# Performance work log

Measured on AMD Instinct MI355X. Metric: run time of the kernel, lower is better.

Reference implementation:

```python
import jax, jax.numpy as jnp
import numpy as np

N = 100000
E = 1600000
NFEAT, NHID, NCLASS = 128, 128, 64


def setup_inputs() -> dict:
    key = jax.random.key(0)
    ks = jax.random.split(key, 8)
    x = jax.random.normal(ks[0], (N, NFEAT), dtype=jnp.float32)
    edge_index = jax.random.randint(ks[1], (2, E), 0, N, dtype=jnp.int32)
    def glorot(k, fan_in, fan_out):
        s = (6.0 / (fan_in + fan_out)) ** 0.5
        return jax.random.uniform(k, (fan_in, fan_out), jnp.float32, -s, s)
    W0 = glorot(ks[2], NFEAT, NHID)
    b0 = jnp.zeros((NHID,), jnp.float32)
    W1 = glorot(ks[3], NHID, NHID)
    b1 = jnp.zeros((NHID,), jnp.float32)
    W2 = glorot(ks[4], NHID, NCLASS)
    b2 = jnp.zeros((NCLASS,), jnp.float32)
    return {"x": x, "edge_index": edge_index, "W0": W0, "b0": b0,
            "W1": W1, "b1": b1, "W2": W2, "b2": b2}


def _normalized_adj(edge_index):
    # add self-loops (SparseTensor.set_diag)
    loops = jnp.arange(N, dtype=edge_index.dtype)
    row = jnp.concatenate([edge_index[0], loops])
    col = jnp.concatenate([edge_index[1], loops])
    ones = jnp.ones(row.shape[0], jnp.float32)
    deg = jax.ops.segment_sum(ones, row, num_segments=N)  # row sums incl. self-loop
    dis = jnp.where(deg > 0, deg ** -0.5, 0.0)
    w = dis[row] * dis[col]  # DAD: D^-1/2 A D^-1/2
    return row, col, w


def _spmm(row, col, w, h):
    # A @ h via gather + segment-sum: [E+N, d] intermediate
    return jax.ops.segment_sum(w[:, None] * h[col], row, num_segments=N)


def reference(x, edge_index, W0, b0, W1, b1, W2, b2):
    row, col, w = _normalized_adj(edge_index)
    h = x
    for Wl, bl, last in ((W0, b0, False), (W1, b1, False), (W2, b2, True)):
        h = _spmm(row, col, w, h @ Wl) + bl  # GCNConv(normalize=False)
        if not last:
            h = jax.nn.relu(h)  # dropout p=0.0 -> identity
    return h
```

## Files before the change

kernel.cpp:

```cpp
#include <hip/hip_runtime.h>


typedef __attribute__((ext_vector_type(8))) short bf16x8;
typedef __attribute__((ext_vector_type(4))) float floatx4;


__device__ inline unsigned short f2bf(float f) {
    union { float f; unsigned u; } v; v.f = f;
    unsigned r = v.u + 0x7fffu + ((v.u >> 16) & 1u);
    return (unsigned short)(r >> 16);
}

__device__ inline float bf2f(unsigned short h) {
    union { unsigned u; float f; } v; v.u = (unsigned)h << 16;
    return v.f;
}

__device__ inline void split_bf(float v, unsigned short& h, unsigned short& l) {
    h = f2bf(v);
    l = f2bf(v - bf2f(h));
}

__device__ inline void bf2x_to_f(unsigned u, float& a, float& b) {
    union { unsigned x; float f; } lo, hi;
    lo.x = u << 16; hi.x = u & 0xffff0000u;
    a = lo.f; b = hi.f;
}

__device__ inline void add8(float* acc, uint4 u) {
    float a, b;
    bf2x_to_f(u.x, a, b); acc[0] += a; acc[1] += b;
    bf2x_to_f(u.y, a, b); acc[2] += a; acc[3] += b;
    bf2x_to_f(u.z, a, b); acc[4] += a; acc[5] += b;
    bf2x_to_f(u.w, a, b); acc[6] += a; acc[7] += b;
}


__global__ void k_count(const int* __restrict__ row, int* __restrict__ deg,
                        int* __restrict__ pos, int e) {
    int i = blockIdx.x * blockDim.x + threadIdx.x;
    if (i < e) pos[i] = atomicAdd(&deg[row[i]], 1);
}

__global__ void k_dis(const int* __restrict__ deg, float* __restrict__ dis, int n) {
    int i = blockIdx.x * blockDim.x + threadIdx.x;
    if (i < n) dis[i] = rsqrtf((float)(deg[i] + 1));
}

__global__ void k_scan1(const int* __restrict__ deg, int* __restrict__ rp,
                        int* __restrict__ bsum, int n) {
    __shared__ int s[256];
    int tid = threadIdx.x;
    int i = blockIdx.x * 256 + tid;
    int v = (i < n) ? deg[i] : 0;
    s[tid] = v;
    __syncthreads();
    for (int off = 1; off < 256; off <<= 1) {
        int t = (tid >= off) ? s[tid - off] : 0;
        __syncthreads();
        s[tid] += t;
        __syncthreads();
    }
    if (i < n) rp[i] = s[tid] - v;
    if (tid == 255) bsum[blockIdx.x] = s[255];
}

__global__ void k_scan2(const int* __restrict__ bsum, int* __restrict__ boffs,
                        int nb, int* __restrict__ rp, int n, int total) {
    __shared__ int s[512];
    int tid = threadIdx.x;
    int v = (tid < nb) ? bsum[tid] : 0;
    s[tid] = v;
    __syncthreads();
    for (int off = 1; off < 512; off <<= 1) {
        int t = (tid >= off) ? s[tid - off] : 0;
        __syncthreads();
        s[tid] += t;
        __syncthreads();
    }
    if (tid < nb) boffs[tid] = s[tid] - v;
    if (tid == 0) rp[n] = total;
}

__global__ void k_scan3(int* __restrict__ rp, const int* __restrict__ boffs, int n) {
    int i = blockIdx.x * blockDim.x + threadIdx.x;
    if (i < n) rp[i] += boffs[i >> 8];
}

__global__ void k_scatter(const int* __restrict__ row, const int* __restrict__ col,
                          const int* __restrict__ rp, const int* __restrict__ pos,
                          int* __restrict__ csr, int e) {
    int i = blockIdx.x * blockDim.x + threadIdx.x;
    if (i < e) {
        int r = row[i];
        csr[rp[r] + pos[i]] = col[i];
    }
}


__global__ void k_prepX(const float* __restrict__ X, unsigned short* __restrict__ Xhi,
                        unsigned short* __restrict__ Xlo, int total4) {
    int id = blockIdx.x * blockDim.x + threadIdx.x;
    if (id < total4) {
        float4 v = ((const float4*)X)[id];
        ushort4 h, l;
        split_bf(v.x, h.x, l.x);
        split_bf(v.y, h.y, l.y);
        split_bf(v.z, h.z, l.z);
        split_bf(v.w, h.w, l.w);
        ((ushort4*)Xhi)[id] = h;
        ((ushort4*)Xlo)[id] = l;
    }
}

__global__ void k_prepW(const float* __restrict__ W, unsigned short* __restrict__ Wthi,
                        unsigned short* __restrict__ Wtlo, int ldw) {
    int id = blockIdx.x * blockDim.x + threadIdx.x;
    if (id < 128 * ldw) {
        int k = id / ldw, nn = id - k * ldw;
        unsigned short h, l;
        split_bf(W[id], h, l);
        Wthi[nn * 128 + k] = h;
        Wtlo[nn * 128 + k] = l;
    }
}


template <int NB>
__global__ __launch_bounds__(256) void k_gemm_mfma(
    const unsigned short* __restrict__ Ahi, const unsigned short* __restrict__ Alo,
    const unsigned short* __restrict__ Wthi, const unsigned short* __restrict__ Wtlo,
    const float* __restrict__ dis, unsigned short* __restrict__ T, int n) {
    const int LDW = NB * 64;
    __shared__ unsigned short Ah_s[64 * 128];
    __shared__ unsigned short Al_s[64 * 128];
    const int tid = threadIdx.x;
    const int bid = blockIdx.x;
    const int bx = (NB == 2) ? (bid >> 1) : bid;
    const int by = (NB == 2) ? (bid & 1) : 0;
    const int row0 = bx * 64;
    const int col0 = by * 64;

    const int wave = tid >> 6, lane = tid & 63;
    const int ln = lane & 15, quad = lane >> 4;
    const int m0 = (wave >> 1) * 32;
    const int nq0 = (wave & 1) * 32;

    bf16x8 Bh[4][2], Bl[4][2];
#pragma unroll
    for (int s = 0; s < 4; s++)
#pragma unroll
        for (int j = 0; j < 2; j++) {
            int ncol = col0 + nq0 + 16 * j + ln;
            int koff = 32 * s + quad * 8;
            Bh[s][j] = *(const bf16x8*)&Wthi[ncol * 128 + koff];
            Bl[s][j] = *(const bf16x8*)&Wtlo[ncol * 128 + koff];
        }

#pragma unroll
    for (int k = 0; k < 4; k++) {
        int id = k * 256 + tid;
        int r = id >> 4, c = id & 15;
        int gr = row0 + r;
        uint4 vh = make_uint4(0, 0, 0, 0), vl = make_uint4(0, 0, 0, 0);
        if (gr < n) {
            vh = *(const uint4*)&Ahi[(size_t)gr * 128 + c * 8];
            vl = *(const uint4*)&Alo[(size_t)gr * 128 + c * 8];
        }
        int pc = c ^ (r & 15);
        *(uint4*)&Ah_s[r * 128 + pc * 8] = vh;
        *(uint4*)&Al_s[r * 128 + pc * 8] = vl;
    }
    __syncthreads();

    floatx4 acc[2][2];
#pragma unroll
    for (int i = 0; i < 2; i++)
#pragma unroll
        for (int j = 0; j < 2; j++) acc[i][j] = (floatx4){0.f, 0.f, 0.f, 0.f};

#pragma unroll
    for (int s = 0; s < 4; s++) {
        bf16x8 ah[2], al[2];
#pragma unroll
        for (int i = 0; i < 2; i++) {
            int off = (m0 + 16 * i + ln) * 128 + ((4 * s + quad) ^ ln) * 8;
            ah[i] = *(const bf16x8*)&Ah_s[off];
            al[i] = *(const bf16x8*)&Al_s[off];
        }
#pragma unroll
        for (int i = 0; i < 2; i++)
#pragma unroll
            for (int j = 0; j < 2; j++) {
                acc[i][j] = __builtin_amdgcn_mfma_f32_16x16x32_bf16(
                    ah[i], Bh[s][j], acc[i][j], 0, 0, 0);
                acc[i][j] = __builtin_amdgcn_mfma_f32_16x16x32_bf16(
                    ah[i], Bl[s][j], acc[i][j], 0, 0, 0);
                acc[i][j] = __builtin_amdgcn_mfma_f32_16x16x32_bf16(
                    al[i], Bh[s][j], acc[i][j], 0, 0, 0);
            }
    }

#pragma unroll
    for (int i = 0; i < 2; i++)
#pragma unroll
        for (int reg = 0; reg < 4; reg++) {
            int gr = row0 + m0 + 16 * i + quad * 4 + reg;
            if (gr < n) {
                float ds = dis[gr];
#pragma unroll
                for (int j = 0; j < 2; j++) {
                    int gc = col0 + nq0 + 16 * j + ln;
                    T[(size_t)gr * LDW + gc] = f2bf(ds * acc[i][j][reg]);
                }
            }
        }
}


__global__ void k_agg128(const unsigned short* __restrict__ T,
                         unsigned short* __restrict__ Ohi,
                         unsigned short* __restrict__ Olo,
                         const int* __restrict__ rp, const int* __restrict__ cols,
                         const float* __restrict__ dis, const float* __restrict__ bias,
                         int n) {
    int wid = (blockIdx.x * blockDim.x + threadIdx.x) >> 6;
    int lane = threadIdx.x & 63;
    if (wid >= n) return;
    const int quad = lane >> 4;
    const int fl = (lane & 15) * 8;
    int beg = rp[wid], end = rp[wid + 1];

    float acc[8] = {0.f, 0.f, 0.f, 0.f, 0.f, 0.f, 0.f, 0.f};
    int e = beg + quad;
    for (; e + 12 < end; e += 16) {
        int c0 = cols[e];
        int c1 = cols[e + 4];
        int c2 = cols[e + 8];
        int c3 = cols[e + 12];
        uint4 u0 = *(const uint4*)&T[(size_t)c0 * 128 + fl];
        uint4 u1 = *(const uint4*)&T[(size_t)c1 * 128 + fl];
        uint4 u2 = *(const uint4*)&T[(size_t)c2 * 128 + fl];
        uint4 u3 = *(const uint4*)&T[(size_t)c3 * 128 + fl];
        add8(acc, u0);
        add8(acc, u1);
        add8(acc, u2);
        add8(acc, u3);
    }
    for (; e < end; e += 4) {
        int c = cols[e];
        uint4 u = *(const uint4*)&T[(size_t)c * 128 + fl];
        add8(acc, u);
    }
#pragma unroll
    for (int k = 0; k < 8; k++) {
        acc[k] += __shfl_xor(acc[k], 16);
        acc[k] += __shfl_xor(acc[k], 32);
    }
    if (quad == 0) {
        uint4 us = *(const uint4*)&T[(size_t)wid * 128 + fl];
        add8(acc, us);
        float di = dis[wid];
        float4 bA = *(const float4*)&bias[fl];
        float4 bB = *(const float4*)&bias[fl + 4];
        float bb[8] = {bA.x, bA.y, bA.z, bA.w, bB.x, bB.y, bB.z, bB.w};
        unsigned short h[8], l[8];
#pragma unroll
        for (int k = 0; k < 8; k++) {
            float o = fmaf(di, acc[k], bb[k]);
            o = fmaxf(o, 0.f);
            split_bf(o, h[k], l[k]);
        }
        ushort4 h0 = {h[0], h[1], h[2], h[3]}, h1 = {h[4], h[5], h[6], h[7]};
        ushort4 l0 = {l[0], l[1], l[2], l[3]}, l1 = {l[4], l[5], l[6], l[7]};
        *(ushort4*)&Ohi[(size_t)wid * 128 + fl] = h0;
        *(ushort4*)&Ohi[(size_t)wid * 128 + fl + 4] = h1;
        *(ushort4*)&Olo[(size_t)wid * 128 + fl] = l0;
        *(ushort4*)&Olo[(size_t)wid * 128 + fl + 4] = l1;
    }
}

__global__ void k_agg64(const unsigned short* __restrict__ T, float* __restrict__ O,
                        const int* __restrict__ rp, const int* __restrict__ cols,
                        const float* __restrict__ dis, const float* __restrict__ bias,
                        int n) {
    int wid = (blockIdx.x * blockDim.x + threadIdx.x) >> 6;
    int lane = threadIdx.x & 63;
    if (wid >= n) return;
    const int oct = lane >> 3;
    const int fl = (lane & 7) * 8;
    int beg = rp[wid], end = rp[wid + 1];

    float acc[8] = {0.f, 0.f, 0.f, 0.f, 0.f, 0.f, 0.f, 0.f};
    int e = beg + oct;
    for (; e + 8 < end; e += 16) {
        int c0 = cols[e];
        int c1 = cols[e + 8];
        uint4 u0 = *(const uint4*)&T[(size_t)c0 * 64 + fl];
        uint4 u1 = *(const uint4*)&T[(size_t)c1 * 64 + fl];
        add8(acc, u0);
        add8(acc, u1);
    }
    if (e < end) {
        int c = cols[e];
        uint4 u = *(const uint4*)&T[(size_t)c * 64 + fl];
        add8(acc, u);
    }
#pragma unroll
    for (int k = 0; k < 8; k++) {
        acc[k] += __shfl_xor(acc[k], 8);
        acc[k] += __shfl_xor(acc[k], 16);
        acc[k] += __shfl_xor(acc[k], 32);
    }
    if (oct == 0) {
        uint4 us = *(const uint4*)&T[(size_t)wid * 64 + fl];
        add8(acc, us);
        float di = dis[wid];
        float4 bA = *(const float4*)&bias[fl];
        float4 bB = *(const float4*)&bias[fl + 4];
        float bb[8] = {bA.x, bA.y, bA.z, bA.w, bB.x, bB.y, bB.z, bB.w};
        float o[8];
#pragma unroll
        for (int k = 0; k < 8; k++)
            o[k] = fmaf(di, acc[k], bb[k]);
        *(float4*)&O[(size_t)wid * 64 + fl] = make_float4(o[0], o[1], o[2], o[3]);
        *(float4*)&O[(size_t)wid * 64 + fl + 4] = make_float4(o[4], o[5], o[6], o[7]);
    }
}


static inline char* align256(char* p) {
    return (char*)(((uintptr_t)p + 255) & ~(uintptr_t)255);
}

extern "C" void kernel_launch(void* const* d_in, const int* in_sizes, int n_in,
                              void* d_out, int out_size, void* d_ws, size_t ws_size,
                              hipStream_t stream) {
    const float* x  = (const float*)d_in[0];
    const int*   ei = (const int*)d_in[1];
    const float* W0 = (const float*)d_in[2];
    const float* b0 = (const float*)d_in[3];
    const float* W1 = (const float*)d_in[4];
    const float* b1 = (const float*)d_in[5];
    const float* W2 = (const float*)d_in[6];
    const float* b2 = (const float*)d_in[7];

    const int Nn = in_sizes[0] / 128;
    const int Ee = in_sizes[1] / 2;
    const int* rowI = ei;
    const int* colI = ei + Ee;

    char* p = (char*)d_ws;
    unsigned short* Tb  = (unsigned short*)p; p += (size_t)Nn * 128 * 2; p = align256(p);
    unsigned short* Ahi = (unsigned short*)p; p += (size_t)Nn * 128 * 2; p = align256(p);
    unsigned short* Alo = (unsigned short*)p; p += (size_t)Nn * 128 * 2; p = align256(p);
    int* csr    = (int*)p;   p += (size_t)Ee * 4;       p = align256(p);
    int* pos    = (int*)p;   p += (size_t)Ee * 4;       p = align256(p);
    int* rp     = (int*)p;   p += (size_t)(Nn + 1) * 4; p = align256(p);
    int* deg    = (int*)p;   p += (size_t)Nn * 4;       p = align256(p);
    float* dis  = (float*)p; p += (size_t)Nn * 4;       p = align256(p);
    int* bsum   = (int*)p;   p += 512 * 4;
    int* boffs  = (int*)p;   p += 512 * 4;
    unsigned short* Wt0h = (unsigned short*)p; p += 128 * 128 * 2;
    unsigned short* Wt0l = (unsigned short*)p; p += 128 * 128 * 2;
    unsigned short* Wt1h = (unsigned short*)p; p += 128 * 128 * 2;
    unsigned short* Wt1l = (unsigned short*)p; p += 128 * 128 * 2;
    unsigned short* Wt2h = (unsigned short*)p; p += 64 * 128 * 2;
    unsigned short* Wt2l = (unsigned short*)p; p += 64 * 128 * 2;

    const int eb = (Ee + 255) / 256;
    const int nb = (Nn + 255) / 256;

    hipMemsetAsync(deg, 0, (size_t)Nn * 4, stream);

    k_count<<<eb, 256, 0, stream>>>(rowI, deg, pos, Ee);
    k_dis<<<nb, 256, 0, stream>>>(deg, dis, Nn);
    k_scan1<<<nb, 256, 0, stream>>>(deg, rp, bsum, Nn);
    k_scan2<<<1, 512, 0, stream>>>(bsum, boffs, nb, rp, Nn, Ee);
    k_scan3<<<nb, 256, 0, stream>>>(rp, boffs, Nn);
    k_scatter<<<eb, 256, 0, stream>>>(rowI, colI, rp, pos, csr, Ee);

    k_prepX<<<(Nn * 32 + 255) / 256, 256, 0, stream>>>(x, Ahi, Alo, Nn * 32);
    k_prepW<<<64, 256, 0, stream>>>(W0, Wt0h, Wt0l, 128);
    k_prepW<<<64, 256, 0, stream>>>(W1, Wt1h, Wt1l, 128);
    k_prepW<<<32, 256, 0, stream>>>(W2, Wt2h, Wt2l, 64);

    const int gx = (Nn + 63) / 64;
    const int ab = (Nn + 3) / 4;

    k_gemm_mfma<2><<<2 * gx, 256, 0, stream>>>(Ahi, Alo, Wt0h, Wt0l, dis, Tb, Nn);
    k_agg128<<<ab, 256, 0, stream>>>(Tb, Ahi, Alo, rp, csr, dis, b0, Nn);
    k_gemm_mfma<2><<<2 * gx, 256, 0, stream>>>(Ahi, Alo, Wt1h, Wt1l, dis, Tb, Nn);
    k_agg128<<<ab, 256, 0, stream>>>(Tb, Ahi, Alo, rp, csr, dis, b1, Nn);
    k_gemm_mfma<1><<<gx, 256, 0, stream>>>(Ahi, Alo, Wt2h, Wt2l, dis, Tb, Nn);
    k_agg64<<<ab, 256, 0, stream>>>(Tb, (float*)d_out, rp, csr, dis, b2, Nn);
}
```

Baseline: 493.2 us.

## Fuse CSR build and prep into one cooperative kernel; rebalance aggregation loops

Replaces the memset plus ten small launches (count, scan phases, scatter, X/W bf16 split) with a single cooperative kernel of 1024 blocks that uses grid-wide syncs between phases. The aim is to remove per-launch overhead and idle gaps between the small preprocessing kernels. The aggregation kernels also change how edges are split across sub-groups: each sub-group now takes a contiguous chunk of the row and processes four edges per iteration, with clamped indices and zero weights masking the tail. The cost is serialization at grid barriers, limited parallelism from the fixed grid size, and redundant masked loads on short rows.

Measured after the change: 950.4 us. 92.7% more time.

```diff
diff --git a/kernel.cpp b/kernel.cpp
--- a/kernel.cpp
+++ b/kernel.cpp
@@ -1,4 +1,7 @@
 #include <hip/hip_runtime.h>
+#include <hip/hip_cooperative_groups.h>
+
+namespace cg = cooperative_groups;
 
 
 typedef __attribute__((ext_vector_type(8))) short bf16x8;
@@ -27,101 +30,118 @@
     a = lo.f; b = hi.f;
 }
 
-__device__ inline void add8(float* acc, uint4 u) {
+__device__ inline void accw8(float* acc, uint4 u, float w) {
     float a, b;
-    bf2x_to_f(u.x, a, b); acc[0] += a; acc[1] += b;
-    bf2x_to_f(u.y, a, b); acc[2] += a; acc[3] += b;
-    bf2x_to_f(u.z, a, b); acc[4] += a; acc[5] += b;
-    bf2x_to_f(u.w, a, b); acc[6] += a; acc[7] += b;
-}
-
-
-__global__ void k_count(const int* __restrict__ row, int* __restrict__ deg,
-                        int* __restrict__ pos, int e) {
-    int i = blockIdx.x * blockDim.x + threadIdx.x;
-    if (i < e) pos[i] = atomicAdd(&deg[row[i]], 1);
-}
-
-__global__ void k_dis(const int* __restrict__ deg, float* __restrict__ dis, int n) {
-    int i = blockIdx.x * blockDim.x + threadIdx.x;
-    if (i < n) dis[i] = rsqrtf((float)(deg[i] + 1));
-}
-
-__global__ void k_scan1(const int* __restrict__ deg, int* __restrict__ rp,
-                        int* __restrict__ bsum, int n) {
-    __shared__ int s[256];
-    int tid = threadIdx.x;
-    int i = blockIdx.x * 256 + tid;
-    int v = (i < n) ? deg[i] : 0;
-    s[tid] = v;
-    __syncthreads();
-    for (int off = 1; off < 256; off <<= 1) {
-        int t = (tid >= off) ? s[tid - off] : 0;
+    bf2x_to_f(u.x, a, b); acc[0] = fmaf(w, a, acc[0]); acc[1] = fmaf(w, b, acc[1]);
+    bf2x_to_f(u.y, a, b); acc[2] = fmaf(w, a, acc[2]); acc[3] = fmaf(w, b, acc[3]);
+    bf2x_to_f(u.z, a, b); acc[4] = fmaf(w, a, acc[4]); acc[5] = fmaf(w, b, acc[5]);
+    bf2x_to_f(u.w, a, b); acc[6] = fmaf(w, a, acc[6]); acc[7] = fmaf(w, b, acc[7]);
+}
+
+
+__global__ __launch_bounds__(256) void k_build(
+    const int* __restrict__ row, const int* __restrict__ col,
+    const float* __restrict__ x,
+    int* __restrict__ deg, int* __restrict__ pos, int* __restrict__ rp,
+    int* __restrict__ csr, float* __restrict__ dis,
+    unsigned short* __restrict__ Ahi, unsigned short* __restrict__ Alo,
+    int* __restrict__ bsum, int* __restrict__ boffs,
+    const float* __restrict__ W0, const float* __restrict__ W1,
+    const float* __restrict__ W2,
+    unsigned short* __restrict__ Wt0h, unsigned short* __restrict__ Wt0l,
+    unsigned short* __restrict__ Wt1h, unsigned short* __restrict__ Wt1l,
+    unsigned short* __restrict__ Wt2h, unsigned short* __restrict__ Wt2l,
+    int n, int e, int nb) {
+    cg::grid_group grid = cg::this_grid();
+    const int tid = threadIdx.x;
+    const int gsz = gridDim.x * blockDim.x;
+    const int gid = blockIdx.x * blockDim.x + tid;
+    __shared__ int s[512];
+
+    for (int i = gid; i < n; i += gsz) deg[i] = 0;
+    grid.sync();
+
+    for (int i = gid; i < e; i += gsz) pos[i] = atomicAdd(&deg[row[i]], 1);
+    grid.sync();
+
+    if (blockIdx.x < nb) {
+        int i = blockIdx.x * 256 + tid;
+        int v = (i < n) ? deg[i] : 0;
+        s[tid] = v;
         __syncthreads();
-        s[tid] += t;
+        for (int off = 1; off < 256; off <<= 1) {
+            int t = (tid >= off) ? s[tid - off] : 0;
+            __syncthreads();
+            s[tid] += t;
+            __syncthreads();
+        }
+        if (i < n) rp[i] = s[tid] - v;
+        if (tid == 255) bsum[blockIdx.x] = s[255];
+    }
+    grid.sync();
+
+    if (blockIdx.x == 0) {
+        int o0 = (tid < nb) ? bsum[tid] : 0;
+        int o1 = (tid + 256 < nb) ? bsum[tid + 256] : 0;
+        s[tid] = o0;
+        s[tid + 256] = o1;
         __syncthreads();
-    }
-    if (i < n) rp[i] = s[tid] - v;
-    if (tid == 255) bsum[blockIdx.x] = s[255];
-}
-
-__global__ void k_scan2(const int* __restrict__ bsum, int* __restrict__ boffs,
-                        int nb, int* __restrict__ rp, int n, int total) {
-    __shared__ int s[512];
-    int tid = threadIdx.x;
-    int v = (tid < nb) ? bsum[tid] : 0;
-    s[tid] = v;
-    __syncthreads();
-    for (int off = 1; off < 512; off <<= 1) {
-        int t = (tid >= off) ? s[tid - off] : 0;
-        __syncthreads();
-        s[tid] += t;
-        __syncthreads();
-    }
-    if (tid < nb) boffs[tid] = s[tid] - v;
-    if (tid == 0) rp[n] = total;
-}
-
-__global__ void k_scan3(int* __restrict__ rp, const int* __restrict__ boffs, int n) {
-    int i = blockIdx.x * blockDim.x + threadIdx.x;
-    if (i < n) rp[i] += boffs[i >> 8];
-}
-
-__global__ void k_scatter(const int* __restrict__ row, const int* __restrict__ col,
-                          const int* __restrict__ rp, const int* __restrict__ pos,
-                          int* __restrict__ csr, int e) {
-    int i = blockIdx.x * blockDim.x + threadIdx.x;
-    if (i < e) {
+        for (int off = 1; off < 256; off <<= 1) {
+            int t = (tid >= off) ? s[tid - off] : 0;
+            __syncthreads();
+            s[tid] += t;
+            __syncthreads();
+        }
+        int t0 = s[255];
+        for (int off = 1; off < 256; off <<= 1) {
+            int t = (tid >= off) ? s[256 + tid - off] : 0;
+            __syncthreads();
+            s[256 + tid] += t;
+            __syncthreads();
+        }
+        boffs[tid] = s[tid] - o0;
+        boffs[256 + tid] = s[256 + tid] + t0 - o1;
+        if (tid == 0) rp[n] = t0 + s[511];
+    }
+    grid.sync();
+
+    for (int i = gid; i < n; i += gsz) {
+        rp[i] += boffs[i >> 8];
+        dis[i] = rsqrtf((float)(deg[i] + 1));
+    }
+    grid.sync();
+
+    for (int i = gid; i < e; i += gsz) {
         int r = row[i];
         csr[rp[r] + pos[i]] = col[i];
     }
-}
-
-
-__global__ void k_prepX(const float* __restrict__ X, unsigned short* __restrict__ Xhi,
-                        unsigned short* __restrict__ Xlo, int total4) {
-    int id = blockIdx.x * blockDim.x + threadIdx.x;
-    if (id < total4) {
-        float4 v = ((const float4*)X)[id];
+    const int total4 = n * 32;
+    for (int id = gid; id < total4; id += gsz) {
+        float4 v = ((const float4*)x)[id];
         ushort4 h, l;
         split_bf(v.x, h.x, l.x);
         split_bf(v.y, h.y, l.y);
         split_bf(v.z, h.z, l.z);
         split_bf(v.w, h.w, l.w);
-        ((ushort4*)Xhi)[id] = h;
-        ((ushort4*)Xlo)[id] = l;
-    }
-}
-
-__global__ void k_prepW(const float* __restrict__ W, unsigned short* __restrict__ Wthi,
-                        unsigned short* __restrict__ Wtlo, int ldw) {
-    int id = blockIdx.x * blockDim.x + threadIdx.x;
-    if (id < 128 * ldw) {
-        int k = id / ldw, nn = id - k * ldw;
+        ((ushort4*)Ahi)[id] = h;
+        ((ushort4*)Alo)[id] = l;
+    }
+    for (int id = gid; id < 128 * 128; id += gsz) {
+        int k = id >> 7, nn = id & 127;
         unsigned short h, l;
-        split_bf(W[id], h, l);
-        Wthi[nn * 128 + k] = h;
-        Wtlo[nn * 128 + k] = l;
+        split_bf(W0[id], h, l);
+        Wt0h[nn * 128 + k] = h;
+        Wt0l[nn * 128 + k] = l;
+        split_bf(W1[id], h, l);
+        Wt1h[nn * 128 + k] = h;
+        Wt1l[nn * 128 + k] = l;
+    }
+    for (int id = gid; id < 128 * 64; id += gsz) {
+        int k = id >> 6, nn = id & 63;
+        unsigned short h, l;
+        split_bf(W2[id], h, l);
+        Wt2h[nn * 128 + k] = h;
+        Wt2l[nn * 128 + k] = l;
     }
 }
 
@@ -230,27 +250,31 @@
     const int quad = lane >> 4;
     const int fl = (lane & 15) * 8;
     int beg = rp[wid], end = rp[wid + 1];
+    int deg = end - beg;
+    int span = (deg + 3) >> 2;
+    int qb = beg + quad * span;
+    int qe = qb + span;
+    if (qe > end) qe = end;
 
     float acc[8] = {0.f, 0.f, 0.f, 0.f, 0.f, 0.f, 0.f, 0.f};
-    int e = beg + quad;
-    for (; e + 12 < end; e += 16) {
+    for (int e = qb; e < qe; e += 4) {
+        int l = qe - 1;
+        int i1 = e + 1, i2 = e + 2, i3 = e + 3;
         int c0 = cols[e];
-        int c1 = cols[e + 4];
-        int c2 = cols[e + 8];
-        int c3 = cols[e + 12];
+        int c1 = cols[i1 < l ? i1 : l];
+        int c2 = cols[i2 < l ? i2 : l];
+        int c3 = cols[i3 < l ? i3 : l];
+        float m1 = (i1 < qe) ? 1.f : 0.f;
+        float m2 = (i2 < qe) ? 1.f : 0.f;
+        float m3 = (i3 < qe) ? 1.f : 0.f;
         uint4 u0 = *(const uint4*)&T[(size_t)c0 * 128 + fl];
         uint4 u1 = *(const uint4*)&T[(size_t)c1 * 128 + fl];
         uint4 u2 = *(const uint4*)&T[(size_t)c2 * 128 + fl];
         uint4 u3 = *(const uint4*)&T[(size_t)c3 * 128 + fl];
-        add8(acc, u0);
-        add8(acc, u1);
-        add8(acc, u2);
-        add8(acc, u3);
-    }
-    for (; e < end; e += 4) {
-        int c = cols[e];
-        uint4 u = *(const uint4*)&T[(size_t)c * 128 + fl];
-        add8(acc, u);
+        accw8(acc, u0, 1.f);
+        accw8(acc, u1, m1);
+        accw8(acc, u2, m2);
+        accw8(acc, u3, m3);
     }
 #pragma unroll
     for (int k = 0; k < 8; k++) {
@@ -259,7 +283,7 @@
     }
     if (quad == 0) {
         uint4 us = *(const uint4*)&T[(size_t)wid * 128 + fl];
-        add8(acc, us);
+        accw8(acc, us, 1.f);
         float di = dis[wid];
         float4 bA = *(const float4*)&bias[fl];
         float4 bB = *(const float4*)&bias[fl + 4];
@@ -290,21 +314,31 @@
     const int oct = lane >> 3;
     const int fl = (lane & 7) * 8;
     int beg = rp[wid], end = rp[wid + 1];
+    int deg = end - beg;
+    int span = (deg + 7) >> 3;
+    int qb = beg + oct * span;
+    int qe = qb + span;
+    if (qe > end) qe = end;
 
     float acc[8] = {0.f, 0.f, 0.f, 0.f, 0.f, 0.f, 0.f, 0.f};
-    int e = beg + oct;
-    for (; e + 8 < end; e += 16) {
+    for (int e = qb; e < qe; e += 4) {
+        int l = qe - 1;
+        int i1 = e + 1, i2 = e + 2, i3 = e + 3;
         int c0 = cols[e];
-        int c1 = cols[e + 8];
+        int c1 = cols[i1 < l ? i1 : l];
+        int c2 = cols[i2 < l ? i2 : l];
+        int c3 = cols[i3 < l ? i3 : l];
+        float m1 = (i1 < qe) ? 1.f : 0.f;
+        float m2 = (i2 < qe) ? 1.f : 0.f;
+        float m3 = (i3 < qe) ? 1.f : 0.f;
         uint4 u0 = *(const uint4*)&T[(size_t)c0 * 64 + fl];
         uint4 u1 = *(const uint4*)&T[(size_t)c1 * 64 + fl];
-        add8(acc, u0);
-        add8(acc, u1);
-    }
-    if (e < end) {
-        int c = cols[e];
-        uint4 u = *(const uint4*)&T[(size_t)c * 64 + fl];
-        add8(acc, u);
+        uint4 u2 = *(const uint4*)&T[(size_t)c2 * 64 + fl];
+        uint4 u3 = *(const uint4*)&T[(size_t)c3 * 64 + fl];
+        accw8(acc, u0, 1.f);
+        accw8(acc, u1, m1);
+        accw8(acc, u2, m2);
+        accw8(acc, u3, m3);
     }
 #pragma unroll
     for (int k = 0; k < 8; k++) {
@@ -314,7 +348,7 @@
     }
     if (oct == 0) {
         uint4 us = *(const uint4*)&T[(size_t)wid * 64 + fl];
-        add8(acc, us);
+        accw8(acc, us, 1.f);
         float di = dis[wid];
         float4 bA = *(const float4*)&bias[fl];
         float4 bB = *(const float4*)&bias[fl + 4];
@@ -345,8 +379,8 @@
     const float* W2 = (const float*)d_in[6];
     const float* b2 = (const float*)d_in[7];
 
-    const int Nn = in_sizes[0] / 128;
-    const int Ee = in_sizes[1] / 2;
+    int Nn = in_sizes[0] / 128;
+    int Ee = in_sizes[1] / 2;
     const int* rowI = ei;
     const int* colI = ei + Ee;
 
@@ -368,22 +402,18 @@
     unsigned short* Wt2h = (unsigned short*)p; p += 64 * 128 * 2;
     unsigned short* Wt2l = (unsigned short*)p; p += 64 * 128 * 2;
 
-    const int eb = (Ee + 255) / 256;
-    const int nb = (Nn + 255) / 256;
-
-    hipMemsetAsync(deg, 0, (size_t)Nn * 4, stream);
-
-    k_count<<<eb, 256, 0, stream>>>(rowI, deg, pos, Ee);
-    k_dis<<<nb, 256, 0, stream>>>(deg, dis, Nn);
-    k_scan1<<<nb, 256, 0, stream>>>(deg, rp, bsum, Nn);
-    k_scan2<<<1, 512, 0, stream>>>(bsum, boffs, nb, rp, Nn, Ee);
-    k_scan3<<<nb, 256, 0, stream>>>(rp, boffs, Nn);
-    k_scatter<<<eb, 256, 0, stream>>>(rowI, colI, rp, pos, csr, Ee);
-
-    k_prepX<<<(Nn * 32 + 255) / 256, 256, 0, stream>>>(x, Ahi, Alo, Nn * 32);
-    k_prepW<<<64, 256, 0, stream>>>(W0, Wt0h, Wt0l, 128);
-    k_prepW<<<64, 256, 0, stream>>>(W1, Wt1h, Wt1l, 128);
-    k_prepW<<<32, 256, 0, stream>>>(W2, Wt2h, Wt2l, 64);
+    int nb = (Nn + 255) / 256;
+
+    void* args[] = {
+        (void*)&rowI, (void*)&colI, (void*)&x,
+        (void*)&deg, (void*)&pos, (void*)&rp, (void*)&csr, (void*)&dis,
+        (void*)&Ahi, (void*)&Alo, (void*)&bsum, (void*)&boffs,
+        (void*)&W0, (void*)&W1, (void*)&W2,
+        (void*)&Wt0h, (void*)&Wt0l, (void*)&Wt1h, (void*)&Wt1l,
+        (void*)&Wt2h, (void*)&Wt2l,
+        (void*)&Nn, (void*)&Ee, (void*)&nb};
+    hipLaunchCooperativeKernel((const void*)k_build, dim3(1024), dim3(256),
+                               args, 0, stream);
 
     const int gx = (Nn + 63) / 64;
     const int ab = (Nn + 3) / 4;
```
